# Performance work log

Measured on AMD Instinct MI355X. Metric: run time of the kernel, lower is better.

Reference implementation:

```python
import jax, jax.numpy as jnp
import numpy as np

E = 65536; N = 10000; LAT = 128; K = 8; OH = 128; GD = 64
M0, M1, M2 = 64, 32, 16                 # multiplicities of 0e, 1o, 2e
D_EDGE = M0 + 3 * M1 + 5 * M2           # 240
NG = M1 + M2                            # 48 gate scalars
O0 = M0 + NG                            # 112 scalar outputs of SO2 (scalars + gates)
C0, C1, C2 = 3 * M0, 3 * M1, 3 * M2     # per-l channels of cat(node, edge, node)
FIN0 = C0 + C1 + C2                     # 336 channels at m=0
FIN1 = C1 + C2                          # 144 channels at |m|=1
FIN2 = C2                               # 48 channels at |m|=2
OUT0 = O0 + M1 + M2                     # 160


def _silu(x):
    return x * jax.nn.sigmoid(x)


def _mlp(x, Ws, bs):
    for i, (W, b) in enumerate(zip(Ws, bs)):
        x = x @ W + b
        if i < len(Ws) - 1:
            x = _silu(x)
    return x


def _split(f):
    # [*, 240] -> scalars [*,64], l1 [*,32,3], l2 [*,16,5]
    return (f[:, :M0],
            f[:, M0:M0 + 3 * M1].reshape(-1, M1, 3),
            f[:, M0 + 3 * M1:].reshape(-1, M2, 5))


def forward(latents, node_features, node_onehot, edge_features, edge_vector,
            cutoff_coeffs, edge_one_hot, wigner_D1, wigner_D2, mole_globals,
            Wg, W0, W1r, W1i, W2r, W2i, P0, b0, P1, P2, We, be, ln_g, ln_b,
            M1W0, M1b0, M1W1, M1b1, M1W2, M1b2,
            M2W0, M2b0, M2W1, M2b1, M2W2, M2b2,
            T0, T1, T2, edge_index, active_edges):
    ec = edge_index[0][active_edges]
    en = edge_index[1][active_edges]
    nc = node_features[ec]
    nnb = node_features[en]
    lat_a = latents[active_edges]

    nc0, nc1, nc2 = _split(nc)
    ef0, ef1, ef2 = _split(edge_features)
    nn0, nn1, nn2 = _split(nnb)
    x0 = jnp.concatenate([nc0, ef0, nn0], 1)          # [E,192]
    x1 = jnp.concatenate([nc1, ef1, nn1], 1)          # [E,96,3]
    x2 = jnp.concatenate([nc2, ef2, nn2], 1)          # [E,48,5]

    # rotate into the edge-aligned frame with cached Wigner D matrices
    y1 = jnp.einsum('eij,ecj->eci', wigner_D1, x1)
    y2 = jnp.einsum('eij,ecj->eci', wigner_D2, x2)

    # expert gates: softmax over routed experts + always-on shared expert
    g = jax.nn.softmax(mole_globals @ Wg, axis=-1)    # [E,K]
    gf = jnp.concatenate([g, jnp.ones((g.shape[0], 1), g.dtype)], 1)  # [E,K+1]

    def moe(f, W):  # f [E,F], W [K+1,F,O] -> gated mixture of expert linears
        return jnp.einsum('eko,ek->eo', jnp.einsum('ef,kfo->eko', f, W), gf)

    # SO(2) linear: independent mixing per |m|
    f0 = jnp.concatenate([x0, y1[:, :, 1], y2[:, :, 2]], 1)   # [E,336]
    o0 = moe(f0, W0)                                          # [E,160]
    o0_s, o0_1, o0_2 = o0[:, :O0], o0[:, O0:O0 + M1], o0[:, O0 + M1:]
    fp1 = jnp.concatenate([y1[:, :, 2], y2[:, :, 3]], 1)      # [E,144]
    fm1 = jnp.concatenate([y1[:, :, 0], y2[:, :, 1]], 1)
    op1 = moe(fp1, W1r) - moe(fm1, W1i)                       # [E,48]
    om1 = moe(fp1, W1i) + moe(fm1, W1r)
    fp2, fm2 = y2[:, :, 4], y2[:, :, 0]                       # [E,48]
    op2 = moe(fp2, W2r) - moe(fm2, W2i)                       # [E,16]
    om2 = moe(fp2, W2i) + moe(fm2, W2r)

    z1 = jnp.stack([om1[:, :M1], o0_1, op1[:, :M1]], -1)      # [E,32,3]
    z2 = jnp.stack([om2, om1[:, M1:], o0_2, op1[:, M1:], op2], -1)  # [E,16,5]
    z1 = jnp.einsum('eji,ecj->eci', wigner_D1, z1)            # rotate back (D^T)
    z2 = jnp.einsum('eji,ecj->eci', wigner_D2, z2)

    # Gate activation: silu scalars, sigmoid gates multiply l>0 parts
    sc = _silu(o0_s[:, :M0])
    gates = jax.nn.sigmoid(o0_s[:, M0:])
    v1 = z1 * gates[:, :M1, None]
    v2 = z2 * gates[:, M1:, None]

    # lin_post: per-l channel mixing, bias on scalars only
    sc = sc @ P0 + b0
    v1 = jnp.einsum('ecm,cd->edm', v1, P1)
    v2 = jnp.einsum('ecm,cd->edm', v2, P2)
    scalars = sc                                              # [E,64]

    # E3ElementLinear: per-channel weights generated from latents
    w = lat_a @ We + be                                       # [E,112]
    sc = sc * w[:, :M0]
    v1 = v1 * w[:, M0:M0 + M1, None]
    v2 = v2 * w[:, M0 + M1:, None]
    new_edge = jnp.concatenate([sc, v1.reshape(-1, 3 * M1), v2.reshape(-1, 5 * M2)], 1)

    # latent update: LN -> MLP1(cat scalars) -> MLP2(cat one-hot) -> cutoff
    mu = lat_a.mean(-1, keepdims=True)
    var = ((lat_a - mu) ** 2).mean(-1, keepdims=True)
    ln = (lat_a - mu) * jax.lax.rsqrt(var + 1e-5) * ln_g + ln_b
    nl = _mlp(jnp.concatenate([ln, scalars], 1), [M1W0, M1W1, M1W2], [M1b0, M1b1, M1b2])
    nl = _mlp(jnp.concatenate([nl, edge_one_hot], 1), [M2W0, M2W1, M2W2], [M2b0, M2b1, M2b2])
    nl = cutoff_coeffs[active_edges][:, None] * nl

    # residual update (identity res since irreps_in == irreps_out)
    upd = jax.nn.sigmoid(jnp.zeros((), new_edge.dtype))
    c_old = jax.lax.rsqrt(upd * upd + 1.0)
    c_new = upd * c_old
    edge_out = c_old * edge_features + c_new * new_edge
    latents = latents.at[active_edges].set(c_new * nl + c_old * lat_a)

    # edge one-hot tensor product (uvu, weighted): per-channel scale from one-hot
    s = 1.0 / jnp.sqrt(jnp.asarray(OH, new_edge.dtype))
    t0 = (edge_one_hot @ T0.T) * s                            # [E,64]
    t1 = (edge_one_hot @ T1.T) * s                            # [E,32]
    t2 = (edge_one_hot @ T2.T) * s                            # [E,16]
    e0, e1, e2 = _split(edge_out)
    oh = jnp.concatenate([e0 * t0,
                          (e1 * t1[:, :, None]).reshape(-1, 3 * M1),
                          (e2 * t2[:, :, None]).reshape(-1, 5 * M2)], 1)
    edge_out = edge_out + oh
    return edge_out, latents, wigner_D1, wigner_D2


def setup_inputs():
    key = jax.random.key(0)
    ks = iter(jax.random.split(key, 64))

    def rn(shape, scale=1.0):
        return jax.random.normal(next(ks), shape, dtype=jnp.float32) * scale

    d = {}
    d['latents'] = rn((E, LAT))
    d['node_features'] = rn((N, D_EDGE))
    d['node_onehot'] = rn((N, GD))
    d['edge_features'] = rn((E, D_EDGE))
    ev = rn((E, 3))
    d['edge_vector'] = ev / jnp.linalg.norm(ev, axis=-1, keepdims=True)
    d['cutoff_coeffs'] = jax.random.uniform(next(ks), (E,), dtype=jnp.float32)
    d['edge_one_hot'] = rn((E, OH))
    d['wigner_D1'] = rn((E, 3, 3), 1.0 / np.sqrt(3))
    d['wigner_D2'] = rn((E, 5, 5), 1.0 / np.sqrt(5))
    d['mole_globals'] = rn((E, GD))
    d['edge_index'] = jax.random.randint(next(ks), (2, E), 0, N, dtype=jnp.int32)
    d['active_edges'] = jnp.arange(E, dtype=jnp.int32)
    # parameters
    d['Wg'] = rn((GD, K), 1.0 / np.sqrt(GD))
    d['W0'] = rn((K + 1, FIN0, OUT0), 1.0 / np.sqrt(FIN0))
    d['W1r'] = rn((K + 1, FIN1, NG), 1.0 / np.sqrt(FIN1))
    d['W1i'] = rn((K + 1, FIN1, NG), 1.0 / np.sqrt(FIN1))
    d['W2r'] = rn((K + 1, FIN2, M2), 1.0 / np.sqrt(FIN2))
    d['W2i'] = rn((K + 1, FIN2, M2), 1.0 / np.sqrt(FIN2))
    d['P0'] = rn((M0, M0), 1.0 / np.sqrt(M0)); d['b0'] = jnp.zeros((M0,), jnp.float32)
    d['P1'] = rn((M1, M1), 1.0 / np.sqrt(M1))
    d['P2'] = rn((M2, M2), 1.0 / np.sqrt(M2))
    d['We'] = rn((LAT, M0 + M1 + M2), 1.0 / np.sqrt(LAT))
    d['be'] = jnp.zeros((M0 + M1 + M2,), jnp.float32)
    d['ln_g'] = jnp.ones((LAT,), jnp.float32); d['ln_b'] = jnp.zeros((LAT,), jnp.float32)
    d['M1W0'] = rn((LAT + M0, 128), 1.0 / np.sqrt(LAT + M0)); d['M1b0'] = jnp.zeros((128,), jnp.float32)
    d['M1W1'] = rn((128, 128), 1.0 / np.sqrt(128)); d['M1b1'] = jnp.zeros((128,), jnp.float32)
    d['M1W2'] = rn((128, LAT), 1.0 / np.sqrt(128)); d['M1b2'] = jnp.zeros((LAT,), jnp.float32)
    d['M2W0'] = rn((LAT + OH, 128), 1.0 / np.sqrt(LAT + OH)); d['M2b0'] = jnp.zeros((128,), jnp.float32)
    d['M2W1'] = rn((128, 128), 1.0 / np.sqrt(128)); d['M2b1'] = jnp.zeros((128,), jnp.float32)
    d['M2W2'] = rn((128, LAT), 1.0 / np.sqrt(128)); d['M2b2'] = jnp.zeros((LAT,), jnp.float32)
    d['T0'] = rn((M0, OH), 1.0 / np.sqrt(OH))
    d['T1'] = rn((M1, OH), 1.0 / np.sqrt(OH))
    d['T2'] = rn((M2, OH), 1.0 / np.sqrt(OH))
    return d


def reference(latents, node_features, node_onehot, edge_features, edge_vector,
              cutoff_coeffs, edge_one_hot, wigner_D1, wigner_D2, mole_globals,
              Wg, W0, W1r, W1i, W2r, W2i, P0, b0, P1, P2, We, be, ln_g, ln_b,
              M1W0, M1b0, M1W1, M1b1, M1W2, M1b2,
              M2W0, M2b0, M2W1, M2b1, M2W2, M2b2,
              T0, T1, T2, edge_index, active_edges):
    return forward(latents, node_features, node_onehot, edge_features, edge_vector,
                   cutoff_coeffs, edge_one_hot, wigner_D1, wigner_D2, mole_globals,
                   Wg, W0, W1r, W1i, W2r, W2i, P0, b0, P1, P2, We, be, ln_g, ln_b,
                   M1W0, M1b0, M1W1, M1b1, M1W2, M1b2,
                   M2W0, M2b0, M2W1, M2b1, M2W2, M2b2,
                   T0, T1, T2, edge_index, active_edges)
```

## Files before the change

kernel.cpp:

```cpp
#include <hip/hip_runtime.h>
#include <hip/hip_bf16.h>
#include <stdint.h>

#define EDGES 65536

typedef unsigned int uint;
typedef unsigned short ushort;
using bf16x8 = __attribute__((ext_vector_type(8))) __bf16;
using f32x4  = __attribute__((ext_vector_type(4))) float;
using uintx4 = __attribute__((ext_vector_type(4))) uint;
using float4v = __attribute__((ext_vector_type(4))) float;
using float2v = __attribute__((ext_vector_type(2))) float;

#define C_OLD 0.8944271909999159f
#define C_NEW 0.4472135954999579f
#define T_SCALE 0.08838834764831845f

__device__ __forceinline__ ushort f2bf(float f) {
  uint x = __builtin_bit_cast(uint, f);
  uint r = x + 0x7FFFu + ((x >> 16) & 1u);
  return (ushort)(r >> 16);
}
__device__ __forceinline__ float bf2f(ushort u) {
  uint x = (uint)u << 16;
  return __builtin_bit_cast(float, x);
}
__device__ __forceinline__ void gload16(const void* g, void* l) {
  __builtin_amdgcn_global_load_lds(
      (const __attribute__((address_space(1))) void*)g,
      (__attribute__((address_space(3))) void*)l, 16, 0, 0);
}

__global__ __launch_bounds__(256) void k_pack_b0(const float* __restrict__ W0, ushort* __restrict__ B) {
  int idx = blockIdx.x * 256 + threadIdx.x;
  if (idx >= 160 * 3456) return;
  int o = idx / 3456, kf = idx - o * 3456;
  int k = kf / 384, f = kf - k * 384;
  float v = (f < 336) ? W0[k * 53760 + f * 160 + o] : 0.f;
  B[idx] = f2bf(v);
}
__global__ __launch_bounds__(256) void k_pack_b1(const float* __restrict__ Wr, const float* __restrict__ Wi, ushort* __restrict__ B) {
  int idx = blockIdx.x * 256 + threadIdx.x;
  if (idx >= 96 * 2880) return;
  int c = idx / 2880, kf = idx - c * 2880;
  int k = kf / 320, f = kf - k * 320;
  float v = 0.f;
  if (f < 288) {
    if (c < 48) v = (f < 144) ? Wr[k * 6912 + f * 48 + c] : -Wi[k * 6912 + (f - 144) * 48 + c];
    else        v = (f < 144) ? Wi[k * 6912 + f * 48 + (c - 48)] : Wr[k * 6912 + (f - 144) * 48 + (c - 48)];
  }
  B[idx] = f2bf(v);
}
__global__ __launch_bounds__(256) void k_pack_b2(const float* __restrict__ Wr, const float* __restrict__ Wi, ushort* __restrict__ B) {
  int idx = blockIdx.x * 256 + threadIdx.x;
  if (idx >= 32 * 1152) return;
  int c = idx / 1152, kf = idx - c * 1152;
  int k = kf / 128, f = kf - k * 128;
  float v = 0.f;
  if (f < 96) {
    if (c < 16) v = (f < 48) ? Wr[k * 768 + f * 16 + c] : -Wi[k * 768 + (f - 48) * 16 + c];
    else        v = (f < 48) ? Wi[k * 768 + f * 16 + (c - 16)] : Wr[k * 768 + (f - 48) * 16 + (c - 16)];
  }
  B[idx] = f2bf(v);
}
struct PackPtrs {
  const float *s0, *s1, *s2, *s3, *s4, *s5, *we, *t0, *t1, *t2, *p0;
  ushort *d0, *d1, *d2, *d3, *d4, *d5, *dwe, *dtt, *dp0;
};
__global__ __launch_bounds__(256) void k_pack_small(PackPtrs p) {
  int idx = blockIdx.x * 256 + threadIdx.x;
  if (idx < 24576) {
    int n = idx / 192, k = idx - n * 192;
    p.d0[idx] = f2bf(p.s0[k * 128 + n]);
  } else if (idx < 40960) {
    int q = idx - 24576; int n = q >> 7, k = q & 127;
    p.d1[q] = f2bf(p.s1[k * 128 + n]);
  } else if (idx < 57344) {
    int q = idx - 40960; int n = q >> 7, k = q & 127;
    p.d2[q] = f2bf(p.s2[k * 128 + n]);
  } else if (idx < 90112) {
    int q = idx - 57344; int n = q / 256, k = q - n * 256;
    p.d3[q] = f2bf(p.s3[k * 128 + n]);
  } else if (idx < 106496) {
    int q = idx - 90112; int n = q >> 7, k = q & 127;
    p.d4[q] = f2bf(p.s4[k * 128 + n]);
  } else if (idx < 122880) {
    int q = idx - 106496; int n = q >> 7, k = q & 127;
    p.d5[q] = f2bf(p.s5[k * 128 + n]);
  } else if (idx < 139264) {
    int q = idx - 122880; int n = q >> 7, k = q & 127;
    p.dwe[q] = f2bf((n < 112) ? p.we[k * 112 + n] : 0.f);
  } else if (idx < 155648) {
    int q = idx - 139264; int o = q >> 7, h = q & 127;
    float v = 0.f;
    if (o < 64) v = p.t0[o * 128 + h];
    else if (o < 96) v = p.t1[(o - 64) * 128 + h];
    else if (o < 112) v = p.t2[(o - 96) * 128 + h];
    p.dtt[q] = f2bf(v);
  } else if (idx < 159744) {
    int q = idx - 155648; int n = q >> 6, k = q & 63;
    p.dp0[q] = f2bf(p.p0[k * 64 + n]);
  }
}

__global__ __launch_bounds__(256) void k_prep(
    const float* __restrict__ node_f, const float* __restrict__ edge_f,
    const float* __restrict__ D1g, const float* __restrict__ D2g,
    const float* __restrict__ mg_g, const float* __restrict__ Wg,
    const float* __restrict__ latg, const float* __restrict__ eohg,
    const int* __restrict__ eidx, const int* __restrict__ act,
    ushort* __restrict__ f_all, float* __restrict__ gf_out,
    ushort* __restrict__ lat_bf, ushort* __restrict__ mlp2_in) {
  __shared__ float sh[4][1244];
  const int w = threadIdx.x >> 6, lane = threadIdx.x & 63;
  const int e = blockIdx.x * 4 + w;
  float* s = sh[w];
  float* s_nc = s;
  float* s_ef = s + 240;
  float* s_nn = s + 480;
  float* s_d1 = s + 720;
  float* s_d2 = s + 729;
  float* s_mg = s + 754;
  float* s_lg = s + 818;
  ushort* row = (ushort*)(s + 828);
  const int ae = act[e];
  const int ec = eidx[ae], en = eidx[EDGES + ae];
  if (lane < 60) {
    ((float4v*)s_nc)[lane] = ((const float4v*)(node_f + (size_t)ec * 240))[lane];
    ((float4v*)s_ef)[lane] = ((const float4v*)(edge_f + (size_t)e * 240))[lane];
    ((float4v*)s_nn)[lane] = ((const float4v*)(node_f + (size_t)en * 240))[lane];
  }
  if (lane < 9)  s_d1[lane] = D1g[e * 9 + lane];
  if (lane < 25) s_d2[lane] = D2g[e * 25 + lane];
  s_mg[lane] = mg_g[e * 64 + lane];
  {
    const float* lp = latg + (size_t)ae * 128;
    float a0 = lp[2 * lane], a1 = lp[2 * lane + 1];
    ((uint*)lat_bf)[(size_t)e * 64 + lane] = (uint)f2bf(a0) | ((uint)f2bf(a1) << 16);
    const float* ep = eohg + (size_t)e * 128;
    a0 = ep[2 * lane]; a1 = ep[2 * lane + 1];
    ((uint*)mlp2_in)[(size_t)e * 128 + 64 + lane] = (uint)f2bf(a0) | ((uint)f2bf(a1) << 16);
  }
  {
    int k = lane & 7, hg = lane >> 3;
    float a = 0.f;
#pragma unroll
    for (int h = 0; h < 8; ++h) a += s_mg[hg * 8 + h] * Wg[(hg * 8 + h) * 8 + k];
    a += __shfl_xor(a, 8);
    a += __shfl_xor(a, 16);
    a += __shfl_xor(a, 32);
    if (lane < 8) s_lg[lane] = a;
  }
  if (lane < 12) {
    float m = s_lg[0];
    for (int j = 1; j < 8; ++j) m = fmaxf(m, s_lg[j]);
    float den = 0.f;
    for (int j = 0; j < 8; ++j) den += __expf(s_lg[j] - m);
    float v = 0.f;
    if (lane < 8) v = __expf(s_lg[lane] - m) / den;
    else if (lane == 8) v = 1.f;
    gf_out[e * 12 + lane] = v;
  }
  row[lane]       = f2bf(s_nc[lane]);
  row[64 + lane]  = f2bf(s_ef[lane]);
  row[128 + lane] = f2bf(s_nn[lane]);
  if (lane < 48) row[336 + lane] = 0;
  if (lane < 32) { row[672 + lane] = 0; row[800 + lane] = 0; }
#pragma unroll
  for (int it = 0; it < 5; ++it) {
    int q = lane + it * 64;
    if (q < 288) {
      int i = q / 96, c = q - i * 96;
      const float* src = (c < 32) ? s_nc : (c < 64) ? s_ef : s_nn;
      int base = 64 + (c & 31) * 3;
      float v = s_d1[i * 3] * src[base] + s_d1[i * 3 + 1] * src[base + 1] + s_d1[i * 3 + 2] * src[base + 2];
      int dst = (i == 0) ? 528 : (i == 1) ? 192 : 384;
      row[dst + c] = f2bf(v);
    }
  }
#pragma unroll
  for (int it = 0; it < 4; ++it) {
    int q = lane + it * 64;
    if (q < 240) {
      int i = q / 48, c = q - i * 48;
      const float* src = (c < 16) ? s_nc : (c < 32) ? s_ef : s_nn;
      int base = 160 + (c & 15) * 5;
      float v = s_d2[i * 5] * src[base] + s_d2[i * 5 + 1] * src[base + 1] +
                s_d2[i * 5 + 2] * src[base + 2] + s_d2[i * 5 + 3] * src[base + 3] +
                s_d2[i * 5 + 4] * src[base + 4];
      int dst = (i == 0) ? 752 : (i == 1) ? 624 : (i == 2) ? 288 : (i == 3) ? 480 : 704;
      row[dst + c] = f2bf(v);
    }
  }
  const uintx4* row4 = (const uintx4*)row;
  uintx4* dst4 = (uintx4*)(f_all + (size_t)e * 832);
#pragma unroll
  for (int it = 0; it < 2; ++it) {
    int q = lane + it * 64;
    if (q < 104) dst4[q] = row4[q];
  }
}

template <int WAVES, int BM, int KZP, int SPG2, int NGRP, int NCOL, int FOFF, int ASTRIDE,
          bool HASBIAS, int EPI>
__device__ __forceinline__ void gemm_dev(
    int bid, char* sm,
    const ushort* __restrict__ A, const ushort* __restrict__ Bt,
    const float* __restrict__ gf, const float* __restrict__ bias,
    ushort* __restrict__ outb, int ob_stride, int ob_off,
    ushort* __restrict__ outb2) {
  constexpr int T = WAVES * 64;
  constexpr int WRS = WAVES / 2;
  constexpr int RPW = BM / WRS;
  constexpr int MI = RPW / 16;
  constexpr int NFW = NCOL / 32;
  constexpr int A_BYTES = BM * 128;
  constexpr int B_BYTES = NCOL * 128;
  constexpr int NT2 = KZP / 64;
  constexpr int AI = (BM * 8) / T;
  constexpr int NB = NCOL * 8;
  constexpr int BI = (NB + T - 1) / T;
  static_assert(NCOL % 32 == 0 && KZP % 64 == 0 && RPW % 16 == 0 && (BM * 8) % T == 0, "geom");
  char* a_lds = sm;
  char* b_lds = sm + 2 * A_BYTES;
  const int tid = threadIdx.x;
  const int lane = tid & 63, w = tid >> 6;
  const int wr = w >> 1, wc = w & 1;
  const int g16 = lane >> 4;
  const int lane15 = lane & 15;
  const int e0 = bid * BM;
  const f32x4 vzero = {0.f, 0.f, 0.f, 0.f};

  float gfr[MI][4];
  auto gf_pref = [&](int gx) {
#pragma unroll
    for (int mi = 0; mi < MI; ++mi)
#pragma unroll
      for (int j = 0; j < 4; ++j)
        gfr[mi][j] = gf[(size_t)(e0 + wr * RPW + mi * 16 + g16 * 4 + j) * 12 + gx];
  };
  if constexpr (NGRP > 1) gf_pref(0);

  const char* aSrc[AI];
#pragma unroll
  for (int it = 0; it < AI; ++it) {
    int q = tid + it * T;
    int r = q >> 3, ch = (q & 7) ^ (r & 7);
    aSrc[it] = (const char*)(A + (size_t)(e0 + r) * ASTRIDE + FOFF) + ch * 16;
  }
  const char* bSrc[BI];
#pragma unroll
  for (int it = 0; it < BI; ++it) {
    int q = tid + it * T;
    if (q < NB) {
      int c = q >> 3, ch = (q & 7) ^ (c & 7);
      bSrc[it] = (const char*)(Bt + (size_t)c * KZP) + ch * 16;
    } else bSrc[it] = nullptr;
  }

  auto stage = [&](int t2, int buf) {
    int aoff = (NGRP > 1) ? (t2 % SPG2) * 128 : t2 * 128;
#pragma unroll
    for (int it = 0; it < AI; ++it)
      gload16(aSrc[it] + aoff, a_lds + buf * A_BYTES + (tid - lane + it * T) * 16);
#pragma unroll
    for (int it = 0; it < BI; ++it) {
      int q = tid + it * T;
      if (q < NB)
        gload16(bSrc[it] + t2 * 128, b_lds + buf * B_BYTES + (tid - lane + it * T) * 16);
    }
  };

  f32x4 accS[MI][NFW], accC[MI][NFW];
#pragma unroll
  for (int mi = 0; mi < MI; ++mi)
#pragma unroll
    for (int n = 0; n < NFW; ++n) { accS[mi][n] = vzero; accC[mi][n] = vzero; }

  stage(0, 0);
  __syncthreads();
  int cur = 0;
  for (int t2 = 0; t2 < NT2; ++t2) {
    if (t2 + 1 < NT2) stage(t2 + 1, cur ^ 1);
    const char* aL = a_lds + cur * A_BYTES;
    const char* bL = b_lds + cur * B_BYTES;
#pragma unroll
    for (int s = 0; s < 2; ++s) {
      bf16x8 a[MI];
#pragma unroll
      for (int mi = 0; mi < MI; ++mi) {
        int rA = wr * RPW + mi * 16 + lane15;
        int slot = (s * 4 + g16) ^ (rA & 7);
        a[mi] = *(const bf16x8*)(aL + rA * 128 + slot * 16);
      }
#pragma unroll
      for (int n = 0; n < NFW; ++n) {
        int cB = (wc * NFW + n) * 16 + lane15;
        int slot = (s * 4 + g16) ^ (cB & 7);
        bf16x8 b = *(const bf16x8*)(bL + cB * 128 + slot * 16);
#pragma unroll
        for (int mi = 0; mi < MI; ++mi) {
          if constexpr (NGRP > 1)
            accC[mi][n] = __builtin_amdgcn_mfma_f32_16x16x32_bf16(a[mi], b, accC[mi][n], 0, 0, 0);
          else
            accS[mi][n] = __builtin_amdgcn_mfma_f32_16x16x32_bf16(a[mi], b, accS[mi][n], 0, 0, 0);
        }
      }
    }
    if constexpr (NGRP > 1) {
      if (t2 % SPG2 == SPG2 - 1) {
        int gx = t2 / SPG2;
#pragma unroll
        for (int mi = 0; mi < MI; ++mi)
#pragma unroll
          for (int n = 0; n < NFW; ++n) {
#pragma unroll
            for (int j = 0; j < 4; ++j) accS[mi][n][j] += gfr[mi][j] * accC[mi][n][j];
            accC[mi][n] = vzero;
          }
        if (gx + 1 < NGRP) gf_pref(gx + 1);
      }
    }
    __syncthreads();
    cur ^= 1;
  }

#pragma unroll
  for (int mi = 0; mi < MI; ++mi) {
    const int row0 = wr * RPW + mi * 16 + g16 * 4;
#pragma unroll
    for (int n = 0; n < NFW; ++n) {
      const int c = (wc * NFW + n) * 16 + lane15;
      float bv = 0.f;
      if constexpr (HASBIAS) bv = bias[c];
#pragma unroll
      for (int j = 0; j < 4; ++j) {
        float v = accS[mi][n][j] + bv;
        const int er = e0 + row0 + j;
        if constexpr (EPI == 1) v = v / (1.f + __expf(-v));
        outb[(size_t)er * ob_stride + ob_off + c] = f2bf(v);
        if constexpr (EPI == 2) {
          if ((wc * NFW + n) * 16 < 64)
            outb2[(size_t)er * 256 + c] = f2bf(v / (1.f + __expf(-v)));
        }
      }
    }
  }
}

template <int WAVES, int BM, int KZP, int SPG2, int NGRP, int NCOL, int FOFF, int ASTRIDE,
          bool HASBIAS, int EPI>
__global__ __launch_bounds__(WAVES * 64) void k_gemm(
    const ushort* __restrict__ A, const ushort* __restrict__ Bt,
    const float* __restrict__ gf, const float* __restrict__ bias,
    ushort* __restrict__ outb, int ob_stride, int ob_off,
    ushort* __restrict__ outb2) {
  __shared__ char sm[2 * BM * 128 + 2 * NCOL * 128 + 16];
  gemm_dev<WAVES, BM, KZP, SPG2, NGRP, NCOL, FOFF, ASTRIDE, HASBIAS, EPI>(
      blockIdx.x, sm, A, Bt, gf, bias, outb, ob_stride, ob_off, outb2);
}

struct Small3Args {
  const ushort *latbf, *Wet, *m2in, *Ttb, *P0t;
  const float* b0;
  ushort *wbuf, *tbuf, *m1in;
};
__global__ __launch_bounds__(256) void k_small3(Small3Args a) {
  __shared__ char sm[49168];
  int bid = blockIdx.x;
  if (bid < 1024) {
    gemm_dev<4, 64, 128, 1, 1, 128, 0, 128, false, 0>(
        bid, sm, a.latbf, a.Wet, nullptr, nullptr, a.wbuf, 128, 0, nullptr);
  } else if (bid < 2048) {
    gemm_dev<4, 64, 128, 1, 1, 128, 128, 256, false, 0>(
        bid - 1024, sm, a.m2in, a.Ttb, nullptr, nullptr, a.tbuf, 128, 0, nullptr);
  } else {
    gemm_dev<4, 64, 64, 1, 1, 64, 0, 256, true, 0>(
        bid - 2048, sm, a.m2in, a.P0t, nullptr, a.b0, a.m1in, 192, 128, nullptr);
  }
}

struct MlpArgs {
  const ushort *m1in, *m2in, *Wt1, *Wt2, *Wt3, *Wt4, *Wt5, *Wt6;
  const float *b1, *b2, *b3, *b4, *b5, *b6;
  const int* act;
  const float *cutg, *latg;
  float* out_lat;
};
__global__ __launch_bounds__(256) void k_mlp(MlpArgs A) {
  __shared__ char sm[61440];
  char* Xa = sm;
  char* Xb = sm + 12288;
  char* Xe = sm + 20480;
  char* W0 = sm + 28672;
  char* W1 = sm + 45056;
  const int tid = threadIdx.x;
  const int lane = tid & 63, w = tid >> 6;
  const int wr = w >> 1, wc = w & 1;
  const int lane15 = lane & 15, g16 = lane >> 4;
  const int e32 = blockIdx.x * 32;
  const f32x4 vzero = {0.f, 0.f, 0.f, 0.f};

  auto stage_w = [&](const ushort* Wt, int K2, int t2, char* dst) {
#pragma unroll
    for (int it = 0; it < 4; ++it) {
      int q = tid + it * 256;
      int c = q >> 3, ch = (q & 7) ^ (c & 7);
      gload16((const char*)Wt + (size_t)c * K2 + t2 * 128 + ch * 16,
              dst + (w + it * 4) * 1024);
    }
  };
  {
#pragma unroll
    for (int it = 0; it < 3; ++it) {
      int q = tid + it * 256;
      int r = q / 24, c24 = q - r * 24;
      int t2 = c24 >> 3, ch = (c24 & 7) ^ (r & 7);
      gload16((const char*)A.m1in + (size_t)(e32 + r) * 384 + t2 * 128 + ch * 16,
              Xa + (w + it * 4) * 1024);
    }
#pragma unroll
    for (int it = 0; it < 2; ++it) {
      int q = tid + it * 256;
      int r = q >> 4, c16 = q & 15;
      int t2 = c16 >> 3, ch = (c16 & 7) ^ (r & 7);
      gload16((const char*)A.m2in + (size_t)(e32 + r) * 512 + 256 + t2 * 128 + ch * 16,
              Xe + (w + it * 4) * 1024);
    }
  }
  stage_w(A.Wt1, 384, 0, W0);
  __syncthreads();

  f32x4 acc[4];
#pragma unroll
  for (int n = 0; n < 4; ++n) acc[n] = vzero;

  auto compute = [&](const char* xin, int xstride, int t2loc, const char* wl) {
#pragma unroll
    for (int s = 0; s < 2; ++s) {
      int row = wr * 16 + lane15;
      bf16x8 a = *(const bf16x8*)(xin + row * xstride + t2loc * 128 + (((s * 4 + g16) ^ (row & 7)) << 4));
#pragma unroll
      for (int n = 0; n < 4; ++n) {
        int cB = wc * 64 + n * 16 + lane15;
        bf16x8 b = *(const bf16x8*)(wl + cB * 128 + (((s * 4 + g16) ^ (cB & 7)) << 4));
        acc[n] = __builtin_amdgcn_mfma_f32_16x16x32_bf16(a, b, acc[n], 0, 0, 0);
      }
    }
  };
  auto epi_x = [&](const float* bias, char* xout, int xstride, bool dosilu) {
#pragma unroll
    for (int n = 0; n < 4; ++n) {
      int c = wc * 64 + n * 16 + lane15;
      float bv = bias[c];
      int ch = (n * 16 + lane15) >> 3;
#pragma unroll
      for (int j = 0; j < 4; ++j) {
        int row = wr * 16 + g16 * 4 + j;
        float v = acc[n][j] + bv;
        if (dosilu) v = v / (1.f + __expf(-v));
        *(ushort*)(xout + row * xstride + wc * 128 + ((ch ^ (row & 7)) << 4) + ((lane15 & 7) << 1)) = f2bf(v);
      }
      acc[n] = vzero;
    }
  };

  stage_w(A.Wt1, 384, 1, W1); compute(Xa, 384, 0, W0); __syncthreads();
  stage_w(A.Wt1, 384, 2, W0); compute(Xa, 384, 1, W1); __syncthreads();
  stage_w(A.Wt2, 256, 0, W1); compute(Xa, 384, 2, W0); epi_x(A.b1, Xb, 256, true); __syncthreads();
  stage_w(A.Wt2, 256, 1, W0); compute(Xb, 256, 0, W1); __syncthreads();
  stage_w(A.Wt3, 256, 0, W1); compute(Xb, 256, 1, W0); epi_x(A.b2, Xa, 384, true); __syncthreads();
  stage_w(A.Wt3, 256, 1, W0); compute(Xa, 384, 0, W1); __syncthreads();
  stage_w(A.Wt4, 512, 0, W1); compute(Xa, 384, 1, W0); epi_x(A.b3, Xb, 256, false); __syncthreads();
  stage_w(A.Wt4, 512, 1, W0); compute(Xb, 256, 0, W1); __syncthreads();
  stage_w(A.Wt4, 512, 2, W1); compute(Xb, 256, 1, W0); __syncthreads();
  stage_w(A.Wt4, 512, 3, W0); compute(Xe, 256, 0, W1); __syncthreads();
  stage_w(A.Wt5, 256, 0, W1); compute(Xe, 256, 1, W0); epi_x(A.b4, Xa, 384, true); __syncthreads();
  stage_w(A.Wt5, 256, 1, W0); compute(Xa, 384, 0, W1); __syncthreads();
  stage_w(A.Wt6, 256, 0, W1); compute(Xa, 384, 1, W0); epi_x(A.b5, Xb, 256, true); __syncthreads();
  stage_w(A.Wt6, 256, 1, W0); compute(Xb, 256, 0, W1); __syncthreads();
  compute(Xb, 256, 1, W0);
#pragma unroll
  for (int n = 0; n < 4; ++n) {
    int c = wc * 64 + n * 16 + lane15;
    float bv = A.b6[c];
#pragma unroll
    for (int j = 0; j < 4; ++j) {
      int row = wr * 16 + g16 * 4 + j;
      int er = e32 + row;
      int ae = A.act[er];
      float v = acc[n][j] + bv;
      A.out_lat[(size_t)ae * 128 + c] = C_NEW * A.cutg[ae] * v + C_OLD * A.latg[(size_t)ae * 128 + c];
    }
  }
}

__global__ __launch_bounds__(512) void k_postf(
    const ushort* __restrict__ moeout,
    const float* __restrict__ D1g, const float* __restrict__ D2g,
    const float* __restrict__ latg, const int* __restrict__ act,
    const float* __restrict__ P1, const float* __restrict__ P2,
    const ushort* __restrict__ wbuf, const float* __restrict__ beg,
    const float* __restrict__ lng, const float* __restrict__ lnb,
    const ushort* __restrict__ tbufp, const float* __restrict__ efg,
    ushort* __restrict__ m1in, float* __restrict__ out_edge) {
  __shared__ float SM[1136 + 8 * 920];
  ushort* Btab = (ushort*)SM;
  float* be_s = SM + 768;
  float* lng_s = SM + 880;
  float* lnb_s = SM + 1008;
  const int t = threadIdx.x;
  const int w = t >> 6, lane = t & 63;
  float* Wp = SM + 1136 + w * 920;
  float* o   = Wp;
  float* row = Wp + 224;
  float* sg  = Wp + 464;
  float* d1  = Wp + 512;
  float* d2  = Wp + 524;
  ushort* wvh = (ushort*)(Wp + 552);
  ushort* tvh = (ushort*)(Wp + 608);
  ushort* tile = (ushort*)(Wp + 664);
  const int e = blockIdx.x * 8 + w;
  const int ae = act[e];
  const f32x4 vzero = {0.f, 0.f, 0.f, 0.f};

  float ef[4];
  ef[0] = efg[(size_t)e * 240 + lane];
  ef[1] = efg[(size_t)e * 240 + 64 + lane];
  ef[2] = efg[(size_t)e * 240 + 128 + lane];
  ef[3] = (lane < 48) ? efg[(size_t)e * 240 + 192 + lane] : 0.f;
  float2v ll = ((const float2v*)(latg + (size_t)ae * 128))[lane];

  if (lane < 28) {
    uintx4 raw = *(const uintx4*)(moeout + (size_t)e * 288 + 64 + lane * 8);
    float* dst = o + lane * 8;
#pragma unroll
    for (int j = 0; j < 4; ++j) {
      uint u = raw[j];
      dst[2 * j] = bf2f((ushort)(u & 0xFFFF));
      dst[2 * j + 1] = bf2f((ushort)(u >> 16));
    }
  }
  if (lane < 14) {
    *(uintx4*)((char*)wvh + lane * 16) = *(const uintx4*)(wbuf + (size_t)e * 128 + lane * 8);
    *(uintx4*)((char*)tvh + lane * 16) = *(const uintx4*)(tbufp + (size_t)e * 128 + lane * 8);
  }
  if (lane < 8) {
    uintx4 raw = *(const uintx4*)(m1in + (size_t)e * 192 + 128 + lane * 8);
    float* dst = row + lane * 8;
#pragma unroll
    for (int j = 0; j < 4; ++j) {
      uint u = raw[j];
      dst[2 * j] = bf2f((ushort)(u & 0xFFFF));
      dst[2 * j + 1] = bf2f((ushort)(u >> 16));
    }
  }
  if (lane < 9)  d1[lane] = D1g[(size_t)e * 9 + lane];
  if (lane < 25) d2[lane] = D2g[(size_t)e * 25 + lane];
  if (lane < 48) sg[lane] = 1.f / (1.f + __expf(-o[lane]));

#pragma unroll
  for (int i = 0; i < 3; ++i) {
    int q = t + i * 512;
    int tbl = q >> 9, idx = q & 511;
    int d = idx >> 5, c = idx & 31;
    float v;
    if (tbl == 0) v = P1[c * 32 + d];
    else if (tbl == 1) v = P1[c * 32 + 16 + d];
    else v = (c < 16) ? P2[c * 16 + d] : 0.f;
    Btab[tbl * 512 + d * 32 + (((c >> 3) ^ (d & 3)) << 3) + (c & 7)] = f2bf(v);
  }
  if (t < 368) {
    if (t < 112) be_s[t] = beg[t];
    else if (t < 240) lng_s[t - 112] = lng[t - 112];
    else lnb_s[t - 240] = lnb[t - 240];
  }

  float sum = ll[0] + ll[1];
  float sq = ll[0] * ll[0] + ll[1] * ll[1];
#pragma unroll
  for (int m = 32; m > 0; m >>= 1) {
    sum += __shfl_xor(sum, m);
    sq += __shfl_xor(sq, m);
  }
  const float mu = sum * (1.f / 128.f);
  const float rs = rsqrtf(sq * (1.f / 128.f) - mu * mu + 1e-5f);

  __syncthreads();

  {
    int i = 2 * lane;
    float l0 = (ll[0] - mu) * rs * lng_s[i] + lnb_s[i];
    float l1 = (ll[1] - mu) * rs * lng_s[i + 1] + lnb_s[i + 1];
    ((uint*)m1in)[(size_t)e * 96 + lane] = (uint)f2bf(l0) | ((uint)f2bf(l1) << 16);
  }
#pragma unroll
  for (int rr = 0; rr < 2; ++rr) {
    int r = lane + rr * 64;
    if (r < 96) {
      int m = r >> 5, c = r & 31;
      float v = d1[m] * o[144 + c] + d1[3 + m] * o[48 + c] + d1[6 + m] * o[96 + c];
      tile[m * 32 + (((c >> 3) ^ (m & 3)) << 3) + (c & 7)] = f2bf(v * sg[c]);
    }
  }
#pragma unroll
  for (int rr = 0; rr < 3; ++rr) {
    int r = lane + rr * 64;
    if (r < 160) {
      int rw = 3 + (r >> 5), c = r & 31;
      ushort hv = 0;
      if (c < 16) {
        int m = rw - 3;
        float v = d2[m] * o[208 + c] + d2[5 + m] * o[176 + c] + d2[10 + m] * o[80 + c] +
                  d2[15 + m] * o[128 + c] + d2[20 + m] * o[192 + c];
        hv = f2bf(v * sg[32 + c]);
      }
      tile[rw * 32 + (((c >> 3) ^ (rw & 3)) << 3) + (c & 7)] = hv;
    }
  }
  {
    const int r15 = lane & 15, g = lane >> 4;
    const int fslot = (g ^ (r15 & 3)) << 3;
    bf16x8 afr = *(const bf16x8*)(tile + r15 * 32 + fslot);
    bf16x8 b1a = *(const bf16x8*)(Btab + r15 * 32 + fslot);
    bf16x8 b1b = *(const bf16x8*)(Btab + 512 + r15 * 32 + fslot);
    bf16x8 b2p = *(const bf16x8*)(Btab + 1024 + r15 * 32 + fslot);
    f32x4 v1a = __builtin_amdgcn_mfma_f32_16x16x32_bf16(afr, b1a, vzero, 0, 0, 0);
    f32x4 v1b = __builtin_amdgcn_mfma_f32_16x16x32_bf16(afr, b1b, vzero, 0, 0, 0);
    f32x4 v2r = __builtin_amdgcn_mfma_f32_16x16x32_bf16(afr, b2p, vzero, 0, 0, 0);
    if (g == 0) {
      float s1 = bf2f(wvh[64 + r15]) + be_s[64 + r15];
      row[64 + r15 * 3 + 0] = v1a[0] * s1;
      row[64 + r15 * 3 + 1] = v1a[1] * s1;
      row[64 + r15 * 3 + 2] = v1a[2] * s1;
      float s2 = bf2f(wvh[80 + r15]) + be_s[80 + r15];
      row[64 + (16 + r15) * 3 + 0] = v1b[0] * s2;
      row[64 + (16 + r15) * 3 + 1] = v1b[1] * s2;
      row[64 + (16 + r15) * 3 + 2] = v1b[2] * s2;
      float s3 = bf2f(wvh[96 + r15]) + be_s[96 + r15];
      row[160 + r15 * 5 + 0] = v2r[3] * s3;
    } else if (g == 1) {
      float s3 = bf2f(wvh[96 + r15]) + be_s[96 + r15];
      row[160 + r15 * 5 + 1] = v2r[0] * s3;
      row[160 + r15 * 5 + 2] = v2r[1] * s3;
      row[160 + r15 * 5 + 3] = v2r[2] * s3;
      row[160 + r15 * 5 + 4] = v2r[3] * s3;
    }
  }
  row[lane] = row[lane] * (bf2f(wvh[lane]) + be_s[lane]);
#pragma unroll
  for (int r = 0; r < 4; ++r) {
    int d = lane + r * 64;
    if (r < 3 || lane < 48) {
      float v = C_OLD * ef[r] + C_NEW * row[d];
      int ti = (d < 64) ? d : (d < 160) ? 64 + (d - 64) / 3 : 96 + (d - 160) / 5;
      float f = bf2f(tvh[ti]) * T_SCALE;
      out_edge[(size_t)e * 240 + d] = v * (1.f + f);
    }
  }
}

extern "C" void kernel_launch(void* const* d_in, const int* in_sizes, int n_in,
                              void* d_out, int out_size, void* d_ws, size_t ws_size,
                              hipStream_t stream) {
  const float* latents = (const float*)d_in[0];
  const float* node_f  = (const float*)d_in[1];
  const float* edge_f  = (const float*)d_in[3];
  const float* cutoff  = (const float*)d_in[5];
  const float* eoh     = (const float*)d_in[6];
  const float* D1      = (const float*)d_in[7];
  const float* D2      = (const float*)d_in[8];
  const float* mg      = (const float*)d_in[9];
  const int*   eidx    = (const int*)d_in[10];
  const int*   act     = (const int*)d_in[11];
  const float* Wg      = (const float*)d_in[12];
  const float* W0      = (const float*)d_in[13];
  const float* W1r     = (const float*)d_in[14];
  const float* W1i     = (const float*)d_in[15];
  const float* W2r     = (const float*)d_in[16];
  const float* W2i     = (const float*)d_in[17];
  const float* P0      = (const float*)d_in[18];
  const float* b0      = (const float*)d_in[19];
  const float* P1      = (const float*)d_in[20];
  const float* P2      = (const float*)d_in[21];
  const float* We      = (const float*)d_in[22];
  const float* be      = (const float*)d_in[23];
  const float* lng     = (const float*)d_in[24];
  const float* lnb     = (const float*)d_in[25];
  const float* M1W0_   = (const float*)d_in[26];
  const float* M1b0_   = (const float*)d_in[27];
  const float* M1W1_   = (const float*)d_in[28];
  const float* M1b1_   = (const float*)d_in[29];
  const float* M1W2_   = (const float*)d_in[30];
  const float* M1b2_   = (const float*)d_in[31];
  const float* M2W0_   = (const float*)d_in[32];
  const float* M2b0_   = (const float*)d_in[33];
  const float* M2W1_   = (const float*)d_in[34];
  const float* M2b1_   = (const float*)d_in[35];
  const float* M2W2_   = (const float*)d_in[36];
  const float* M2b2_   = (const float*)d_in[37];
  const float* T0      = (const float*)d_in[38];
  const float* T1      = (const float*)d_in[39];
  const float* T2      = (const float*)d_in[40];

  float* out_edge = (float*)d_out;
  float* out_lat  = out_edge + (size_t)EDGES * 240;
  float* out_d1   = out_lat + (size_t)EDGES * 128;
  float* out_d2   = out_d1 + (size_t)EDGES * 9;

  char* ws = (char*)d_ws;
  size_t off = 0;
  auto alloc = [&](size_t bytes) -> char* {
    char* p = ws + off;
    off += (bytes + 255) & ~size_t(255);
    return p;
  };
  ushort* f_all  = (ushort*)alloc((size_t)EDGES * 832 * 2);
  float*  gfb    = (float*) alloc((size_t)EDGES * 12 * 4);
  ushort* moeout = (ushort*)alloc((size_t)EDGES * 288 * 2);
  ushort* m2in   = (ushort*)alloc((size_t)EDGES * 256 * 2);
  ushort* latbf  = (ushort*)alloc((size_t)EDGES * 128 * 2);
  ushort* wbuf   = (ushort*)alloc((size_t)EDGES * 128 * 2);
  ushort* B0t    = (ushort*)alloc(160 * 3456 * 2);
  ushort* B1t    = (ushort*)alloc(96 * 2880 * 2);
  ushort* B2t    = (ushort*)alloc(32 * 1152 * 2);
  ushort* Wt1    = (ushort*)alloc(128 * 192 * 2);
  ushort* Wt2    = (ushort*)alloc(128 * 128 * 2);
  ushort* Wt3    = (ushort*)alloc(128 * 128 * 2);
  ushort* Wt4    = (ushort*)alloc(128 * 256 * 2);
  ushort* Wt5    = (ushort*)alloc(128 * 128 * 2);
  ushort* Wt6    = (ushort*)alloc(128 * 128 * 2);
  ushort* Wet    = (ushort*)alloc(128 * 128 * 2);
  ushort* Ttb    = (ushort*)alloc(128 * 128 * 2);
  ushort* P0t    = (ushort*)alloc(64 * 64 * 2);

  ushort* m1in = f_all;
  ushort* tbuf = latbf;

  hipMemcpyAsync(out_d1, (const void*)D1, (size_t)EDGES * 9 * 4, hipMemcpyDeviceToDevice, stream);
  hipMemcpyAsync(out_d2, (const void*)D2, (size_t)EDGES * 25 * 4, hipMemcpyDeviceToDevice, stream);

  if (ws_size < off) return;

  k_pack_b0<<<2160, 256, 0, stream>>>(W0, B0t);
  k_pack_b1<<<1080, 256, 0, stream>>>(W1r, W1i, B1t);
  k_pack_b2<<<144, 256, 0, stream>>>(W2r, W2i, B2t);
  PackPtrs pp = {M1W0_, M1W1_, M1W2_, M2W0_, M2W1_, M2W2_, We, T0, T1, T2, P0,
                 Wt1, Wt2, Wt3, Wt4, Wt5, Wt6, Wet, Ttb, P0t};
  k_pack_small<<<624, 256, 0, stream>>>(pp);

  k_prep<<<EDGES / 4, 256, 0, stream>>>(node_f, edge_f, D1, D2, mg, Wg, latents, eoh,
                                        eidx, act, f_all, gfb, latbf, m2in);

  k_gemm<8, 128, 3456, 6, 9, 160, 0, 832, false, 2>
      <<<512, 512, 0, stream>>>(f_all, B0t, gfb, nullptr, moeout, 288, 0, m2in);
  k_gemm<8, 128, 2880, 5, 9, 96, 384, 832, false, 0>
      <<<512, 512, 0, stream>>>(f_all, B1t, gfb, nullptr, moeout, 288, 160, nullptr);
  k_gemm<8, 128, 1152, 2, 9, 32, 704, 832, false, 0>
      <<<512, 512, 0, stream>>>(f_all, B2t, gfb, nullptr, moeout, 288, 256, nullptr);

  Small3Args s3 = {latbf, Wet, m2in, Ttb, P0t, b0, wbuf, tbuf, m1in};
  k_small3<<<3072, 256, 0, stream>>>(s3);

  k_postf<<<EDGES / 8, 512, 0, stream>>>(moeout, D1, D2, latents, act, P1, P2,
                                         wbuf, be, lng, lnb, tbuf, edge_f, m1in, out_edge);

  MlpArgs ma = {m1in, m2in, Wt1, Wt2, Wt3, Wt4, Wt5, Wt6,
                M1b0_, M1b1_, M1b2_, M2b0_, M2b1_, M2b2_,
                act, cutoff, latents, out_lat};
  k_mlp<<<EDGES / 32, 256, 0, stream>>>(ma);
}
```

Before: 452.5 us.

## Keep A fragments in registers for gated expert GEMM instead of re-staging via LDS

For the multi-group (expert-gated) GEMM path, the A tile for one group is loaded once directly from global memory into registers and reused across all expert groups. Only B is double-buffered through LDS. This removes redundant A reloads and LDS traffic per group and shrinks shared memory, which may allow higher occupancy. It costs more registers for the held A fragments, and the direct global loads of A are not staged through LDS.

```diff
diff --git a/kernel.cpp b/kernel.cpp
--- a/kernel.cpp
+++ b/kernel.cpp
@@ -221,33 +221,14 @@
   constexpr int NB = NCOL * 8;
   constexpr int BI = (NB + T - 1) / T;
   static_assert(NCOL % 32 == 0 && KZP % 64 == 0 && RPW % 16 == 0 && (BM * 8) % T == 0, "geom");
-  char* a_lds = sm;
-  char* b_lds = sm + 2 * A_BYTES;
   const int tid = threadIdx.x;
-  const int lane = tid & 63, w = tid >> 6;
-  const int wr = w >> 1, wc = w & 1;
+  const int lane = tid & 63, wid = tid >> 6;
+  const int wr = wid >> 1, wc = wid & 1;
   const int g16 = lane >> 4;
   const int lane15 = lane & 15;
   const int e0 = bid * BM;
   const f32x4 vzero = {0.f, 0.f, 0.f, 0.f};
 
-  float gfr[MI][4];
-  auto gf_pref = [&](int gx) {
-#pragma unroll
-    for (int mi = 0; mi < MI; ++mi)
-#pragma unroll
-      for (int j = 0; j < 4; ++j)
-        gfr[mi][j] = gf[(size_t)(e0 + wr * RPW + mi * 16 + g16 * 4 + j) * 12 + gx];
-  };
-  if constexpr (NGRP > 1) gf_pref(0);
-
-  const char* aSrc[AI];
-#pragma unroll
-  for (int it = 0; it < AI; ++it) {
-    int q = tid + it * T;
-    int r = q >> 3, ch = (q & 7) ^ (r & 7);
-    aSrc[it] = (const char*)(A + (size_t)(e0 + r) * ASTRIDE + FOFF) + ch * 16;
-  }
   const char* bSrc[BI];
 #pragma unroll
   for (int it = 0; it < BI; ++it) {
@@ -258,71 +239,136 @@
     } else bSrc[it] = nullptr;
   }
 
-  auto stage = [&](int t2, int buf) {
-    int aoff = (NGRP > 1) ? (t2 % SPG2) * 128 : t2 * 128;
-#pragma unroll
-    for (int it = 0; it < AI; ++it)
-      gload16(aSrc[it] + aoff, a_lds + buf * A_BYTES + (tid - lane + it * T) * 16);
-#pragma unroll
-    for (int it = 0; it < BI; ++it) {
+  f32x4 accS[MI][NFW];
+#pragma unroll
+  for (int mi = 0; mi < MI; ++mi)
+#pragma unroll
+    for (int n = 0; n < NFW; ++n) accS[mi][n] = vzero;
+
+  if constexpr (NGRP > 1) {
+    char* b_lds = sm;
+    f32x4 accC[MI][NFW];
+#pragma unroll
+    for (int mi = 0; mi < MI; ++mi)
+#pragma unroll
+      for (int n = 0; n < NFW; ++n) accC[mi][n] = vzero;
+
+    float gfr[MI][4];
+    auto gf_pref = [&](int gx) {
+#pragma unroll
+      for (int mi = 0; mi < MI; ++mi)
+#pragma unroll
+        for (int j = 0; j < 4; ++j)
+          gfr[mi][j] = gf[(size_t)(e0 + wr * RPW + mi * 16 + g16 * 4 + j) * 12 + gx];
+    };
+    gf_pref(0);
+
+    bf16x8 afr[SPG2][MI][2];
+#pragma unroll
+    for (int wi = 0; wi < SPG2; ++wi)
+#pragma unroll
+      for (int mi = 0; mi < MI; ++mi)
+#pragma unroll
+        for (int s = 0; s < 2; ++s)
+          afr[wi][mi][s] = *(const bf16x8*)(
+              A + (size_t)(e0 + wr * RPW + mi * 16 + lane15) * ASTRIDE + FOFF +
+              wi * 64 + s * 32 + g16 * 8);
+
+    auto stageB = [&](int t2, int buf) {
+#pragma unroll
+      for (int it = 0; it < BI; ++it) {
+        int q = tid + it * T;
+        if (q < NB)
+          gload16(bSrc[it] + (size_t)t2 * 128, b_lds + buf * B_BYTES + (tid - lane + it * T) * 16);
+      }
+    };
+
+    stageB(0, 0);
+    __syncthreads();
+    int cur = 0;
+    for (int g = 0; g < NGRP; ++g) {
+#pragma unroll
+      for (int wi = 0; wi < SPG2; ++wi) {
+        int t2 = g * SPG2 + wi;
+        if (t2 + 1 < NT2) stageB(t2 + 1, cur ^ 1);
+        const char* bL = b_lds + cur * B_BYTES;
+#pragma unroll
+        for (int s = 0; s < 2; ++s) {
+#pragma unroll
+          for (int n = 0; n < NFW; ++n) {
+            int cB = (wc * NFW + n) * 16 + lane15;
+            int slot = (s * 4 + g16) ^ (cB & 7);
+            bf16x8 b = *(const bf16x8*)(bL + cB * 128 + slot * 16);
+#pragma unroll
+            for (int mi = 0; mi < MI; ++mi)
+              accC[mi][n] = __builtin_amdgcn_mfma_f32_16x16x32_bf16(afr[wi][mi][s], b, accC[mi][n], 0, 0, 0);
+          }
+        }
+        if (wi == SPG2 - 1) {
+#pragma unroll
+          for (int mi = 0; mi < MI; ++mi)
+#pragma unroll
+            for (int n = 0; n < NFW; ++n) {
+#pragma unroll
+              for (int j = 0; j < 4; ++j) accS[mi][n][j] += gfr[mi][j] * accC[mi][n][j];
+              accC[mi][n] = vzero;
+            }
+          if (g + 1 < NGRP) gf_pref(g + 1);
+        }
+        __syncthreads();
+        cur ^= 1;
+      }
+    }
+  } else {
+    char* a_lds = sm;
+    char* b_lds = sm + 2 * A_BYTES;
+    const char* aSrc[AI];
+#pragma unroll
+    for (int it = 0; it < AI; ++it) {
       int q = tid + it * T;
-      if (q < NB)
-        gload16(bSrc[it] + t2 * 128, b_lds + buf * B_BYTES + (tid - lane + it * T) * 16);
-    }
-  };
-
-  f32x4 accS[MI][NFW], accC[MI][NFW];
-#pragma unroll
-  for (int mi = 0; mi < MI; ++mi)
-#pragma unroll
-    for (int n = 0; n < NFW; ++n) { accS[mi][n] = vzero; accC[mi][n] = vzero; }
-
-  stage(0, 0);
-  __syncthreads();
-  int cur = 0;
-  for (int t2 = 0; t2 < NT2; ++t2) {
-    if (t2 + 1 < NT2) stage(t2 + 1, cur ^ 1);
-    const char* aL = a_lds + cur * A_BYTES;
-    const char* bL = b_lds + cur * B_BYTES;
-#pragma unroll
-    for (int s = 0; s < 2; ++s) {
-      bf16x8 a[MI];
-#pragma unroll
-      for (int mi = 0; mi < MI; ++mi) {
-        int rA = wr * RPW + mi * 16 + lane15;
-        int slot = (s * 4 + g16) ^ (rA & 7);
-        a[mi] = *(const bf16x8*)(aL + rA * 128 + slot * 16);
+      int r = q >> 3, ch = (q & 7) ^ (r & 7);
+      aSrc[it] = (const char*)(A + (size_t)(e0 + r) * ASTRIDE + FOFF) + ch * 16;
+    }
+    auto stage = [&](int t2, int buf) {
+#pragma unroll
+      for (int it = 0; it < AI; ++it)
+        gload16(aSrc[it] + t2 * 128, a_lds + buf * A_BYTES + (tid - lane + it * T) * 16);
+#pragma unroll
+      for (int it = 0; it < BI; ++it) {
+        int q = tid + it * T;
+        if (q < NB)
+          gload16(bSrc[it] + t2 * 128, b_lds + buf * B_BYTES + (tid - lane + it * T) * 16);
       }
-#pragma unroll
-      for (int n = 0; n < NFW; ++n) {
-        int cB = (wc * NFW + n) * 16 + lane15;
-        int slot = (s * 4 + g16) ^ (cB & 7);
-        bf16x8 b = *(const bf16x8*)(bL + cB * 128 + slot * 16);
+    };
+    stage(0, 0);
+    __syncthreads();
+    int cur = 0;
+    for (int t2 = 0; t2 < NT2; ++t2) {
+      if (t2 + 1 < NT2) stage(t2 + 1, cur ^ 1);
+      const char* aL = a_lds + cur * A_BYTES;
+      const char* bL = b_lds + cur * B_BYTES;
+#pragma unroll
+      for (int s = 0; s < 2; ++s) {
+        bf16x8 a[MI];
 #pragma unroll
         for (int mi = 0; mi < MI; ++mi) {
-          if constexpr (NGRP > 1)
-            accC[mi][n] = __builtin_amdgcn_mfma_f32_16x16x32_bf16(a[mi], b, accC[mi][n], 0, 0, 0);
-          else
+          int rA = wr * RPW + mi * 16 + lane15;
+          int slot = (s * 4 + g16) ^ (rA & 7);
+          a[mi] = *(const bf16x8*)(aL + rA * 128 + slot * 16);
+        }
+#pragma unroll
+        for (int n = 0; n < NFW; ++n) {
+          int cB = (wc * NFW + n) * 16 + lane15;
+          int slot = (s * 4 + g16) ^ (cB & 7);
+          bf16x8 b = *(const bf16x8*)(bL + cB * 128 + slot * 16);
+#pragma unroll
+          for (int mi = 0; mi < MI; ++mi)
             accS[mi][n] = __builtin_amdgcn_mfma_f32_16x16x32_bf16(a[mi], b, accS[mi][n], 0, 0, 0);
         }
       }
-    }
-    if constexpr (NGRP > 1) {
-      if (t2 % SPG2 == SPG2 - 1) {
-        int gx = t2 / SPG2;
-#pragma unroll
-        for (int mi = 0; mi < MI; ++mi)
-#pragma unroll
-          for (int n = 0; n < NFW; ++n) {
-#pragma unroll
-            for (int j = 0; j < 4; ++j) accS[mi][n][j] += gfr[mi][j] * accC[mi][n][j];
-            accC[mi][n] = vzero;
-          }
-        if (gx + 1 < NGRP) gf_pref(gx + 1);
-      }
-    }
-    __syncthreads();
-    cur ^= 1;
+      __syncthreads();
+      cur ^= 1;
+    }
   }
 
 #pragma unroll
@@ -355,7 +401,7 @@
     const float* __restrict__ gf, const float* __restrict__ bias,
     ushort* __restrict__ outb, int ob_stride, int ob_off,
     ushort* __restrict__ outb2) {
-  __shared__ char sm[2 * BM * 128 + 2 * NCOL * 128 + 16];
+  __shared__ char sm[(NGRP > 1 ? 0 : 2 * BM * 128) + 2 * NCOL * 128 + 16];
   gemm_dev<WAVES, BM, KZP, SPG2, NGRP, NCOL, FOFF, ASTRIDE, HASBIAS, EPI>(
       blockIdx.x, sm, A, Bt, gf, bias, outb, ob_stride, ob_off, outb2);
 }
```

Measured after the change: 448.7 us. About the same (-0.8%).
